# Kernel tuning notes

Hardware: AMD Instinct MI355X
Metric: run time of the kernel (lower is better)

The kernel has to match this reference:

```python
import jax, jax.numpy as jnp
import numpy as np
from jax import lax

B, L = 2048, 2048
CIN, CONV, D, NCLS = 1, 128, 1024, 1000
E, H, K = 6, 2 * 1024, 2  # num_experts, expert hidden, top-k


def setup_inputs() -> dict:
    key = jax.random.key(0)
    ks = jax.random.split(key, 16)
    s = lambda *sh: 0.02
    return {
        "x": jax.random.normal(ks[0], (B, L), jnp.float32),
        "conv1_w": jax.random.normal(ks[1], (CONV, CIN, 5), jnp.float32) * 0.1,
        "conv1_b": jnp.zeros((CONV,), jnp.float32),
        "conv2_w": jax.random.normal(ks[2], (CONV, CONV, 5), jnp.float32) * 0.05,
        "conv2_b": jnp.zeros((CONV,), jnp.float32),
        "proj_w": jax.random.normal(ks[3], (D, CONV), jnp.float32) * 0.05,
        "proj_b": jnp.zeros((D,), jnp.float32),
        "router_w": jax.random.normal(ks[4], (E, D), jnp.float32) * 0.02,
        "router_b": jnp.zeros((E,), jnp.float32),
        "exp_w1": jax.random.normal(ks[5], (E, H, D), jnp.float32) * 0.02,
        "exp_b1": jnp.zeros((E, H), jnp.float32),
        "exp_w2": jax.random.normal(ks[6], (E, D, H), jnp.float32) * 0.02,
        "exp_b2": jnp.zeros((E, D), jnp.float32),
        "cls_w": jax.random.normal(ks[7], (NCLS, D), jnp.float32) * 0.02,
        "cls_b": jnp.zeros((NCLS,), jnp.float32),
    }


def _conv1d(x, w, b):
    # x: [B, C, L]; torch Conv1d(k=5, stride=2, pad=2)
    y = lax.conv_general_dilated(x, w, window_strides=(2,), padding=[(2, 2)],
                                 dimension_numbers=("NCH", "OIH", "NCH"))
    return y + b[None, :, None]


def reference(x, conv1_w, conv1_b, conv2_w, conv2_b, proj_w, proj_b,
              router_w, router_b, exp_w1, exp_b1, exp_w2, exp_b2, cls_w, cls_b):
    h = x[:, None, :]                               # [B,1,L]
    h = jax.nn.relu(_conv1d(h, conv1_w, conv1_b))   # [B,CONV,L/2]
    h = jax.nn.relu(_conv1d(h, conv2_w, conv2_b))   # [B,CONV,L/4]
    h = h.mean(axis=-1)                             # [B,CONV]
    h = h @ proj_w.T + proj_b                       # [B,D]

    # Top-2 router
    probs = jax.nn.softmax(h @ router_w.T + router_b, axis=-1)  # [B,E]
    top_vals, top_idx = lax.top_k(probs, K)                     # [B,2]
    # per-token per-expert combine weights (exact same math as masked loop)
    combine = (jax.nn.one_hot(top_idx[:, 0], E, dtype=h.dtype) * top_vals[:, 0:1]
               + jax.nn.one_hot(top_idx[:, 1], E, dtype=h.dtype) * top_vals[:, 1:2])  # [B,E]

    # all-expert FFN, then masked combine (equivalent to gather/scatter dispatch)
    hid = jax.nn.relu(jnp.einsum("bd,ehd->beh", h, exp_w1) + exp_b1)  # [B,E,H]
    eo = jnp.einsum("beh,edh->bed", hid, exp_w2) + exp_b2             # [B,E,D]
    moe = jnp.einsum("be,bed->bd", combine, eo)                       # [B,D]

    return moe @ cls_w.T + cls_b                                      # [B,NCLS]
```

## Files before the change

### kernel.cpp

```cpp
#include <hip/hip_runtime.h>
#include <hip/hip_bf16.h>
#include <hip/hip_fp16.h>
#include <stdint.h>

#define BB 2048
#define LL 2048
#define CV 128
#define DD 1024
#define NC 1000
#define EE 6
#define HH 2048

typedef __bf16 bf16_t;
typedef _Float16 f16_t;
typedef __attribute__((ext_vector_type(8))) __bf16 bf16x8;
typedef __attribute__((ext_vector_type(8))) _Float16 f16x8;
typedef __attribute__((ext_vector_type(4))) _Float16 f16x4;
typedef __attribute__((ext_vector_type(4))) float f32x4;

__device__ __forceinline__ void gload_lds16(const void* g, void* l)
{
    __builtin_amdgcn_global_load_lds(
        (const __attribute__((address_space(1))) unsigned int*)g,
        (__attribute__((address_space(3))) unsigned int*)l, 16, 0, 0);
}

__global__ void k_prep_w2(const float* __restrict__ w2, bf16_t* __restrict__ wsw)
{
    int idx = blockIdx.x * 256 + threadIdx.x;
    if (idx >= 5 * 128 * 128) return;
    int kk = idx % 5;
    int t2 = idx / 5;
    int ci = t2 & 127;
    int co = t2 >> 7;
    float v = w2[idx];
    bf16_t h = (bf16_t)v;
    bf16_t l = (bf16_t)(v - (float)h);
    int cb = ci >> 5, j = ci & 31;
    int t  = cb * 5 + kk;
    int si = (co * 32 + j) ^ ((co & 7) << 3);
    wsw[(size_t)t * 8192 + si]        = h;
    wsw[(size_t)t * 8192 + 4096 + si] = l;
}

__global__ void k_prep_exp(const float* __restrict__ ew1, const float* __restrict__ ew2,
                           const float* __restrict__ cw,  f16_t* __restrict__ ew1h,
                           f16_t* __restrict__ ew2h, f16_t* __restrict__ clsh)
{
    const size_t n1 = (size_t)EE * HH * DD / 4;
    const size_t n2 = n1 + (size_t)EE * DD * HH / 4;
    const size_t n3 = n2 + (size_t)NC * DD / 4;
    size_t i4 = (size_t)blockIdx.x * 256 + threadIdx.x;
    if (i4 >= n3) return;
    const float* src; f16_t* dst; size_t off;
    if (i4 < n1)      { src = ew1; dst = ew1h; off = i4; }
    else if (i4 < n2) { src = ew2; dst = ew2h; off = i4 - n1; }
    else              { src = cw;  dst = clsh; off = i4 - n2; }
    float4 v = reinterpret_cast<const float4*>(src)[off];
    f16x4 r;
    r[0] = (f16_t)v.x; r[1] = (f16_t)v.y; r[2] = (f16_t)v.z; r[3] = (f16_t)v.w;
    reinterpret_cast<f16x4*>(dst)[off] = r;
}

__launch_bounds__(512, 2)
__global__ void k_conv(const float* __restrict__ x,  const float* __restrict__ w1,
                       const float* __restrict__ b1, const bf16_t* __restrict__ wsw,
                       const float* __restrict__ b2, float* __restrict__ hbar)
{
    __shared__ __align__(16) float w1s[640];
    __shared__ __align__(16) float b1s[128];
    __shared__ __align__(16) float b2s[128];
    __shared__ __align__(16) float red[8][64];
    __shared__ __align__(16) short h1s[2][2][8320];
    __shared__ __align__(16) short wlds[3 * 8192];

    const int tid  = threadIdx.x;
    const int b0   = blockIdx.x * 2;
    const int lane = tid & 63;
    const int wid  = tid >> 6;
    const int l15  = lane & 15, lg = lane >> 4;
    const int wb   = wid >> 2;
    const int wm   = (wid >> 1) & 1;
    const int wn   = wid & 1;
    const int gb   = tid >> 8;
    const int gtid = tid & 255;
    const int jo   = gtid & 3;
    const int rg   = gtid >> 2;

    for (int i = tid; i < 640; i += 512) w1s[i] = w1[i];
    if (tid < 128) { b1s[tid] = b1[tid]; b2s[tid] = b2[tid]; }

    const float* xrow = x + (size_t)(b0 + gb) * LL;
    const short* h1p  = &h1s[wb][0][0];

    float racc[4][4];
#pragma unroll
    for (int m = 0; m < 4; ++m)
#pragma unroll
        for (int r = 0; r < 4; ++r) racc[m][r] = 0.f;

#define KSTEP(kk, buf)                                                          \
    do {                                                                        \
        const short* wp = wlds + (buf) * 8192;                                  \
        bf16x8 ah[4], al[4], bh[4], bl[4];                                      \
        _Pragma("unroll")                                                       \
        for (int m = 0; m < 4; ++m) {                                           \
            int si = ((wm * 64 + m * 16 + l15) * 32 + lg * 8) ^ ((l15 & 7) << 3); \
            ah[m] = *reinterpret_cast<const bf16x8*>(wp + si);                  \
            al[m] = *reinterpret_cast<const bf16x8*>(wp + 4096 + si);           \
        }                                                                       \
        _Pragma("unroll")                                                       \
        for (int n = 0; n < 4; ++n) {                                           \
            int r = 2 * (wn * 64 + n * 16 + l15) + (kk);                        \
            int si = (r * 32 + lg * 8) ^ (((r >> 1) & 7) << 3);                 \
            bh[n] = *reinterpret_cast<const bf16x8*>(h1p + si);                 \
            bl[n] = *reinterpret_cast<const bf16x8*>(h1p + 8320 + si);          \
        }                                                                       \
        _Pragma("unroll")                                                       \
        for (int m = 0; m < 4; ++m)                                             \
            _Pragma("unroll")                                                   \
            for (int n = 0; n < 4; ++n)                                         \
                acc[m][n] = __builtin_amdgcn_mfma_f32_16x16x32_bf16(ah[m], bh[n], acc[m][n], 0, 0, 0); \
        _Pragma("unroll")                                                       \
        for (int m = 0; m < 4; ++m)                                             \
            _Pragma("unroll")                                                   \
            for (int n = 0; n < 4; ++n)                                         \
                acc[m][n] = __builtin_amdgcn_mfma_f32_16x16x32_bf16(ah[m], bl[n], acc[m][n], 0, 0, 0); \
        _Pragma("unroll")                                                       \
        for (int m = 0; m < 4; ++m)                                             \
            _Pragma("unroll")                                                   \
            for (int n = 0; n < 4; ++n)                                         \
                acc[m][n] = __builtin_amdgcn_mfma_f32_16x16x32_bf16(al[m], bh[n], acc[m][n], 0, 0, 0); \
    } while (0)

    for (int c = 0; c < 4; ++c) {
        const int t1base = 256 * c - 2;

        f32x4 acc[4][4];
#pragma unroll
        for (int m = 0; m < 4; ++m)
#pragma unroll
            for (int n = 0; n < 4; ++n)
#pragma unroll
                for (int r = 0; r < 4; ++r) acc[m][n][r] = 0.f;

        for (int cb = 0; cb < 4; ++cb) {
            __syncthreads();

            {
                const bf16_t* src = wsw + (size_t)cb * 40960;
#pragma unroll
                for (int j = 0; j < 6; ++j) {
                    int q = j * 512 + tid;
                    gload_lds16(src + q * 8, wlds + q * 8);
                }
            }

            const int ci0 = cb * 32 + jo * 8;
            float wf[40], br8[8];
#pragma unroll
            for (int q = 0; q < 10; ++q)
                *reinterpret_cast<float4*>(&wf[q * 4]) =
                    *reinterpret_cast<const float4*>(&w1s[ci0 * 5 + q * 4]);
            *reinterpret_cast<float4*>(&br8[0]) = *reinterpret_cast<const float4*>(&b1s[ci0]);
            *reinterpret_cast<float4*>(&br8[4]) = *reinterpret_cast<const float4*>(&b1s[ci0 + 4]);

#pragma unroll
            for (int it = 0; it < 5; ++it) {
                int r = rg + it * 64;
                if (it < 4 || r < 260) {
                    int t1 = t1base + r;
                    bool valid = (unsigned)t1 < 1024u;
                    float xv[5];
#pragma unroll
                    for (int kk = 0; kk < 5; ++kk) {
                        int xg = 2 * t1 - 2 + kk;
                        xv[kk] = (valid && (unsigned)xg < 2048u) ? xrow[xg] : 0.f;
                    }
                    bf16x8 hv, lv;
#pragma unroll
                    for (int u = 0; u < 8; ++u) {
                        float v = 0.f;
                        if (valid) {
                            v = br8[u];
#pragma unroll
                            for (int kk = 0; kk < 5; ++kk) v += wf[u * 5 + kk] * xv[kk];
                            v = fmaxf(v, 0.f);
                        }
                        bf16_t h = (bf16_t)v;
                        hv[u] = h;
                        lv[u] = (bf16_t)(v - (float)h);
                    }
                    int si = (r * 32 + jo * 8) ^ (((r >> 1) & 7) << 3);
                    *reinterpret_cast<bf16x8*>(&h1s[gb][0][si]) = hv;
                    *reinterpret_cast<bf16x8*>(&h1s[gb][1][si]) = lv;
                }
            }
            __syncthreads();

            KSTEP(0, 0);
            KSTEP(1, 1);
            __syncthreads();

            {
                const bf16_t* src = wsw + (size_t)cb * 40960 + 24576;
#pragma unroll
                for (int j = 0; j < 4; ++j) {
                    int q = j * 512 + tid;
                    gload_lds16(src + q * 8, wlds + q * 8);
                }
            }
            KSTEP(2, 2);
            __syncthreads();

            KSTEP(3, 0);
            KSTEP(4, 1);
        }
#pragma unroll
        for (int m = 0; m < 4; ++m)
#pragma unroll
            for (int r = 0; r < 4; ++r) {
                int co = wm * 64 + m * 16 + lg * 4 + r;
                float bias = b2s[co];
                float s = 0.f;
#pragma unroll
                for (int n = 0; n < 4; ++n) s += fmaxf(acc[m][n][r] + bias, 0.f);
                racc[m][r] += s;
            }
    }
#undef KSTEP

#pragma unroll
    for (int m = 0; m < 4; ++m)
#pragma unroll
        for (int r = 0; r < 4; ++r) {
            float v = racc[m][r];
            v += __shfl_xor(v, 1);
            v += __shfl_xor(v, 2);
            v += __shfl_xor(v, 4);
            v += __shfl_xor(v, 8);
            racc[m][r] = v;
        }
    if (l15 == 0) {
#pragma unroll
        for (int m = 0; m < 4; ++m)
#pragma unroll
            for (int r = 0; r < 4; ++r)
                red[wid][m * 16 + lg * 4 + r] = racc[m][r];
    }
    __syncthreads();
    if (tid < 256) {
        int wb2 = tid >> 7, cc = tid & 127;
        int wm2 = cc >> 6, loc = cc & 63;
        float s = red[wb2 * 4 + wm2 * 2 + 0][loc] + red[wb2 * 4 + wm2 * 2 + 1][loc];
        hbar[(size_t)(b0 + wb2) * 128 + cc] = s * (1.f / 512.f);
    }
}

__launch_bounds__(256)
__global__ void k_proj(const float* __restrict__ hbar, const float* __restrict__ pw,
                       const float* __restrict__ pb, float* __restrict__ h)
{
    __shared__ float hbs[64 * 128];
    const int tid = threadIdx.x;
    const int b0 = blockIdx.x * 64, d0 = blockIdx.y * 64;
    for (int i = tid * 4; i < 64 * 128; i += 1024)
        *reinterpret_cast<float4*>(&hbs[i]) =
            *reinterpret_cast<const float4*>(&hbar[(size_t)b0 * 128 + i]);
    __syncthreads();
    const int tx = tid & 15, ty = tid >> 4;
    float acc[4][4];
#pragma unroll
    for (int i = 0; i < 4; ++i)
#pragma unroll
        for (int j = 0; j < 4; ++j) acc[i][j] = 0.f;
    const float* pwr[4];
#pragma unroll
    for (int j = 0; j < 4; ++j) pwr[j] = pw + (size_t)(d0 + tx * 4 + j) * 128;
    for (int k = 0; k < 128; k += 4) {
        float4 wv[4], av[4];
#pragma unroll
        for (int j = 0; j < 4; ++j) wv[j] = *reinterpret_cast<const float4*>(pwr[j] + k);
#pragma unroll
        for (int i = 0; i < 4; ++i) av[i] = *reinterpret_cast<const float4*>(&hbs[(ty * 4 + i) * 128 + k]);
#pragma unroll
        for (int i = 0; i < 4; ++i)
#pragma unroll
            for (int j = 0; j < 4; ++j)
                acc[i][j] += av[i].x * wv[j].x + av[i].y * wv[j].y +
                             av[i].z * wv[j].z + av[i].w * wv[j].w;
    }
#pragma unroll
    for (int i = 0; i < 4; ++i) {
        int bb = b0 + ty * 4 + i;
#pragma unroll
        for (int j = 0; j < 4; ++j) {
            int d = d0 + tx * 4 + j;
            h[(size_t)bb * DD + d] = acc[i][j] + pb[d];
        }
    }
}

__launch_bounds__(256)
__global__ void k_router(const float* __restrict__ h, const float* __restrict__ rw,
                         const float* __restrict__ rb, float* __restrict__ comb,
                         int2* __restrict__ top)
{
    const int lane = threadIdx.x & 63;
    const int b = blockIdx.x * 4 + (threadIdx.x >> 6);
    float part[6] = {0.f, 0.f, 0.f, 0.f, 0.f, 0.f};
    for (int j = 0; j < 16; ++j) {
        int d = j * 64 + lane;
        float hv = h[(size_t)b * DD + d];
#pragma unroll
        for (int e = 0; e < 6; ++e) part[e] += rw[e * DD + d] * hv;
    }
#pragma unroll
    for (int e = 0; e < 6; ++e) {
        float v = part[e];
        for (int off = 32; off > 0; off >>= 1) v += __shfl_xor(v, off);
        part[e] = v;
    }
    if (lane == 0) {
        float lgt[6];
#pragma unroll
        for (int e = 0; e < 6; ++e) lgt[e] = part[e] + rb[e];
        int i1 = 0;
#pragma unroll
        for (int e = 1; e < 6; ++e) if (lgt[e] > lgt[i1]) i1 = e;
        int i2 = -1;
#pragma unroll
        for (int e = 0; e < 6; ++e)
            if (e != i1 && (i2 < 0 || lgt[e] > lgt[i2])) i2 = e;
        float mx = lgt[i1], s = 0.f, ex[6];
#pragma unroll
        for (int e = 0; e < 6; ++e) { ex[e] = expf(lgt[e] - mx); s += ex[e]; }
        float inv = 1.f / s;
#pragma unroll
        for (int e = 0; e < 6; ++e) comb[b * 8 + e] = 0.f;
        comb[b * 8 + 6] = 0.f; comb[b * 8 + 7] = 0.f;
        comb[b * 8 + i1] = ex[i1] * inv;
        comb[b * 8 + i2] = ex[i2] * inv;
        top[b] = make_int2(i1, i2);
    }
}

__global__ void k_index(const int2* __restrict__ top, int* __restrict__ meta,
                        int* __restrict__ idxg)
{
    __shared__ int wsum[4];
    const int tid = threadIdx.x, lane = tid & 63, wid = tid >> 6;
    int2 tk[8];
#pragma unroll
    for (int j = 0; j < 8; ++j) tk[j] = top[tid * 8 + j];
    int off_run = 0;
    for (int e = 0; e < 6; ++e) {
        int m[8], c = 0;
#pragma unroll
        for (int j = 0; j < 8; ++j) { m[j] = (tk[j].x == e || tk[j].y == e) ? 1 : 0; c += m[j]; }
        int v = c;
        for (int d = 1; d < 64; d <<= 1) { int u = __shfl_up(v, d); if (lane >= d) v += u; }
        if (lane == 63) wsum[wid] = v;
        __syncthreads();
        int wbase = 0;
#pragma unroll
        for (int w = 0; w < 4; ++w) if (w < wid) wbase += wsum[w];
        int total = wsum[0] + wsum[1] + wsum[2] + wsum[3];
        int p = off_run + wbase + (v - c);
#pragma unroll
        for (int j = 0; j < 8; ++j) if (m[j]) idxg[p++] = tid * 8 + j;
        if (tid == 0) { meta[e] = total; meta[8 + e] = off_run; }
        off_run += total;
        __syncthreads();
    }
    if (tid == 0) meta[14] = off_run;
}

__device__ inline f16x8 cvt8(const float4 a, const float4 b)
{
    f16x8 r;
    r[0] = (f16_t)a.x; r[1] = (f16_t)a.y; r[2] = (f16_t)a.z; r[3] = (f16_t)a.w;
    r[4] = (f16_t)b.x; r[5] = (f16_t)b.y; r[6] = (f16_t)b.z; r[7] = (f16_t)b.w;
    return r;
}

template<int EPI, int NFRAG>
__launch_bounds__(256, 3)
__global__ void k_moe(const float* __restrict__ hsrc, const f16_t* __restrict__ hidg,
                      const f16_t* __restrict__ eog, const float* __restrict__ Bp,
                      const f16_t* __restrict__ Bh, const float* __restrict__ bias,
                      f16_t* __restrict__ outH, f16_t* __restrict__ eogW,
                      float* __restrict__ outF, const float* __restrict__ comb,
                      const int2* __restrict__ top, const int* __restrict__ meta,
                      const int* __restrict__ idxg, int N, int K, int NCLIP)
{
    constexpr int BN = NFRAG * 32;
    __shared__ f16_t As[128 * 72];
    __shared__ f16_t Bs[BN * 72];
    const int tid = threadIdx.x;
    const int e  = blockIdx.z;
    const int m0 = blockIdx.x * 128, n0 = blockIdx.y * BN;
    int cnt = 1 << 30, off = 0;
    if (EPI != 3) {
        cnt = meta[e]; off = meta[8 + e];
        if (m0 >= cnt) return;
    }
    const int lane = tid & 63, wid = tid >> 6;
    const int l15 = lane & 15, lg = lane >> 4;
    const int wm = wid >> 1, wn = wid & 1;

    f32x4 acc[4][NFRAG];
#pragma unroll
    for (int i = 0; i < 4; ++i)
#pragma unroll
        for (int j = 0; j < NFRAG; ++j)
#pragma unroll
            for (int r = 0; r < 4; ++r) acc[i][j][r] = 0.f;

    for (int k0 = 0; k0 < K; k0 += 64) {
        __syncthreads();
        {
            const int row = tid >> 1, c0 = (tid & 1) * 32;
            f16x8* d = reinterpret_cast<f16x8*>(As + row * 72 + c0);
            if (EPI == 1) {
                int lr = m0 + row;
                int token = (lr < cnt) ? idxg[off + lr] : 0;
                const float4* s = reinterpret_cast<const float4*>(hsrc + (size_t)token * K + k0 + c0);
#pragma unroll
                for (int j = 0; j < 4; ++j) d[j] = cvt8(s[2 * j], s[2 * j + 1]);
            } else if (EPI == 2) {
                const uint4* s = reinterpret_cast<const uint4*>(hidg + (size_t)(off + m0 + row) * K + k0 + c0);
#pragma unroll
                for (int j = 0; j < 4; ++j) reinterpret_cast<uint4*>(d)[j] = s[j];
            } else {
                int r = m0 + row;
                const f16x8* s0 = reinterpret_cast<const f16x8*>(eog + ((size_t)r * 2) * K + k0 + c0);
                const f16x8* s1 = reinterpret_cast<const f16x8*>(eog + ((size_t)r * 2 + 1) * K + k0 + c0);
#pragma unroll
                for (int j = 0; j < 4; ++j) d[j] = s0[j] + s1[j];
            }
        }
        {
            constexpr int PERTHR = BN * 64 / 256;
            constexpr int TPR = 64 / PERTHR;
            const int row = tid / TPR, c0 = (tid % TPR) * PERTHR;
            const bool ok = (n0 + row) < NCLIP;
            f16x8* d = reinterpret_cast<f16x8*>(Bs + row * 72 + c0);
            if (Bh) {
                const uint4* s = reinterpret_cast<const uint4*>(
                    Bh + (size_t)e * N * K + (size_t)(n0 + row) * K + k0 + c0);
#pragma unroll
                for (int j = 0; j < PERTHR / 8; ++j) {
                    uint4 v = ok ? s[j] : make_uint4(0, 0, 0, 0);
                    reinterpret_cast<uint4*>(d)[j] = v;
                }
            } else {
                const float4* s = reinterpret_cast<const float4*>(
                    Bp + (size_t)e * N * K + (size_t)(n0 + row) * K + k0 + c0);
#pragma unroll
                for (int j = 0; j < PERTHR / 8; ++j) {
                    float4 a = ok ? s[2 * j]     : make_float4(0.f, 0.f, 0.f, 0.f);
                    float4 b = ok ? s[2 * j + 1] : make_float4(0.f, 0.f, 0.f, 0.f);
                    d[j] = cvt8(a, b);
                }
            }
        }
        __syncthreads();
#pragma unroll
        for (int kk = 0; kk < 64; kk += 32) {
            f16x8 af[4], bq[NFRAG];
#pragma unroll
            for (int i = 0; i < 4; ++i)
                af[i] = *reinterpret_cast<const f16x8*>(As + (wm * 64 + i * 16 + l15) * 72 + kk + lg * 8);
#pragma unroll
            for (int j = 0; j < NFRAG; ++j)
                bq[j] = *reinterpret_cast<const f16x8*>(Bs + (wn * (BN / 2) + j * 16 + l15) * 72 + kk + lg * 8);
#pragma unroll
            for (int i = 0; i < 4; ++i)
#pragma unroll
                for (int j = 0; j < NFRAG; ++j)
                    acc[i][j] = __builtin_amdgcn_mfma_f32_16x16x32_f16(af[i], bq[j], acc[i][j], 0, 0, 0);
        }
    }
#pragma unroll
    for (int i = 0; i < 4; ++i) {
#pragma unroll
        for (int j = 0; j < NFRAG; ++j) {
#pragma unroll
            for (int r = 0; r < 4; ++r) {
                int lr  = m0 + wm * 64 + i * 16 + lg * 4 + r;
                int col = n0 + wn * (BN / 2) + j * 16 + l15;
                float c = acc[i][j][r];
                if (EPI == 1) {
                    if (lr < cnt)
                        outH[(size_t)(off + lr) * N + col] = (f16_t)fmaxf(c + bias[(size_t)e * N + col], 0.f);
                } else if (EPI == 2) {
                    if (lr < cnt) {
                        int token = idxg[off + lr];
                        int slot = (top[token].x == e) ? 0 : 1;
                        float w = comb[token * 8 + e];
                        eogW[((size_t)token * 2 + slot) * N + col] = (f16_t)(w * (c + bias[(size_t)e * N + col]));
                    }
                } else {
                    if (col < NCLIP)
                        outF[(size_t)lr * NCLIP + col] = c + bias[col];
                }
            }
        }
    }
}

extern "C" void kernel_launch(void* const* d_in, const int* in_sizes, int n_in,
                              void* d_out, int out_size, void* d_ws, size_t ws_size,
                              hipStream_t stream)
{
    const float* x   = (const float*)d_in[0];
    const float* w1  = (const float*)d_in[1];
    const float* b1  = (const float*)d_in[2];
    const float* w2  = (const float*)d_in[3];
    const float* b2  = (const float*)d_in[4];
    const float* pw  = (const float*)d_in[5];
    const float* pb  = (const float*)d_in[6];
    const float* rw  = (const float*)d_in[7];
    const float* rb  = (const float*)d_in[8];
    const float* ew1 = (const float*)d_in[9];
    const float* eb1 = (const float*)d_in[10];
    const float* ew2 = (const float*)d_in[11];
    const float* eb2 = (const float*)d_in[12];
    const float* cw  = (const float*)d_in[13];
    const float* cb  = (const float*)d_in[14];
    float* out = (float*)d_out;

    char* ws = (char*)d_ws;
    bf16_t* wsw  = (bf16_t*)(ws + 0);
    float*  hbar = (float*)(ws + 327680);
    float*  h    = (float*)(ws + 1376256);
    f16_t*  eog  = (f16_t*)(ws + 1376256);
    float*  comb = (float*)(ws + 9764864);
    int2*   top  = (int2*)(ws + 9830400);
    int*    meta = (int*)(ws + 9846784);
    int*    idxg = (int*)(ws + 9847040);
    f16_t*  hidg = (f16_t*)(ws + 9863424);
    f16_t*  ew1h = (f16_t*)(ws + 27164928);
    f16_t*  ew2h = (f16_t*)(ws + 52330752);
    f16_t*  clsh = (f16_t*)(ws + 77496576);

    const bool f16w = ws_size >= 79593728ull;

    k_prep_w2<<<320, 256, 0, stream>>>(w2, wsw);
    if (f16w)
        k_prep_exp<<<25576, 256, 0, stream>>>(ew1, ew2, cw, ew1h, ew2h, clsh);
    k_conv<<<1024, 512, 0, stream>>>(x, w1, b1, wsw, b2, hbar);
    k_proj<<<dim3(32, 16), 256, 0, stream>>>(hbar, pw, pb, h);
    k_router<<<512, 256, 0, stream>>>(h, rw, rb, comb, top);
    k_index<<<1, 256, 0, stream>>>(top, meta, idxg);
    k_moe<1, 4><<<dim3(16, 16, 6), 256, 0, stream>>>(
        h, nullptr, nullptr, ew1, f16w ? ew1h : nullptr, eb1,
        hidg, nullptr, nullptr, comb, top, meta, idxg, HH, DD, HH);
    k_moe<2, 4><<<dim3(16, 8, 6), 256, 0, stream>>>(
        nullptr, hidg, nullptr, ew2, f16w ? ew2h : nullptr, eb2,
        nullptr, eog, nullptr, comb, top, meta, idxg, DD, HH, DD);
    k_moe<3, 2><<<dim3(16, 16, 1), 256, 0, stream>>>(
        nullptr, nullptr, eog, cw, f16w ? clsh : nullptr, cb,
        nullptr, nullptr, out, comb, top, meta, idxg, DD, DD, NC);
}
```

Before: 731.1 us.

## Switch conv2 MFMA to 32x32x16 tiles and stage input rows in LDS

The conv2 GEMM inside k_conv moves from 16x16x32 bf16 MFMA to 32x32x16 bf16 MFMA. Fragment loads, accumulator layout, the bias/ReLU/mean epilogue and the cross-lane reduction are remapped to fit the new tile shape. The input row chunk for each c-iteration is now loaded once into shared memory, so the conv1 stage reads x from LDS instead of doing repeated guarded global loads. The change adds LDS usage and reworks index mapping, which risks layout mistakes and changes in register pressure.

New measurement: 758.5 us. 1.04x slower.

```diff
diff --git a/kernel.cpp b/kernel.cpp
--- a/kernel.cpp
+++ b/kernel.cpp
@@ -17,6 +17,7 @@
 typedef __attribute__((ext_vector_type(8))) _Float16 f16x8;
 typedef __attribute__((ext_vector_type(4))) _Float16 f16x4;
 typedef __attribute__((ext_vector_type(4))) float f32x4;
+typedef __attribute__((ext_vector_type(16))) float f32x16;
 
 __device__ __forceinline__ void gload_lds16(const void* g, void* l)
 {
@@ -71,6 +72,7 @@
     __shared__ __align__(16) float b1s[128];
     __shared__ __align__(16) float b2s[128];
     __shared__ __align__(16) float red[8][64];
+    __shared__ __align__(16) float xs[2][528];
     __shared__ __align__(16) short h1s[2][2][8320];
     __shared__ __align__(16) short wlds[3 * 8192];
 
@@ -78,7 +80,8 @@
     const int b0   = blockIdx.x * 2;
     const int lane = tid & 63;
     const int wid  = tid >> 6;
-    const int l15  = lane & 15, lg = lane >> 4;
+    const int l31  = lane & 31;
+    const int lh   = lane >> 5;
     const int wb   = wid >> 2;
     const int wm   = (wid >> 1) & 1;
     const int wn   = wid & 1;
@@ -90,59 +93,83 @@
     for (int i = tid; i < 640; i += 512) w1s[i] = w1[i];
     if (tid < 128) { b1s[tid] = b1[tid]; b2s[tid] = b2[tid]; }
 
-    const float* xrow = x + (size_t)(b0 + gb) * LL;
-    const short* h1p  = &h1s[wb][0][0];
-
-    float racc[4][4];
-#pragma unroll
-    for (int m = 0; m < 4; ++m)
-#pragma unroll
-        for (int r = 0; r < 4; ++r) racc[m][r] = 0.f;
+    const short* h1p = &h1s[wb][0][0];
+
+    float racc[2][16];
+#pragma unroll
+    for (int m = 0; m < 2; ++m)
+#pragma unroll
+        for (int g = 0; g < 16; ++g) racc[m][g] = 0.f;
 
 #define KSTEP(kk, buf)                                                          \
     do {                                                                        \
         const short* wp = wlds + (buf) * 8192;                                  \
-        bf16x8 ah[4], al[4], bh[4], bl[4];                                      \
+        bf16x8 ah[2][2], al[2][2], bh[2][2], bl[2][2];                          \
         _Pragma("unroll")                                                       \
-        for (int m = 0; m < 4; ++m) {                                           \
-            int si = ((wm * 64 + m * 16 + l15) * 32 + lg * 8) ^ ((l15 & 7) << 3); \
-            ah[m] = *reinterpret_cast<const bf16x8*>(wp + si);                  \
-            al[m] = *reinterpret_cast<const bf16x8*>(wp + 4096 + si);           \
+        for (int m = 0; m < 2; ++m) {                                           \
+            int co = wm * 64 + m * 32 + l31;                                    \
+            _Pragma("unroll")                                                   \
+            for (int kh = 0; kh < 2; ++kh) {                                    \
+                int si = (co * 32 + kh * 16 + lh * 8) ^ ((co & 7) << 3);        \
+                ah[m][kh] = *reinterpret_cast<const bf16x8*>(wp + si);          \
+                al[m][kh] = *reinterpret_cast<const bf16x8*>(wp + 4096 + si);   \
+            }                                                                   \
         }                                                                       \
         _Pragma("unroll")                                                       \
-        for (int n = 0; n < 4; ++n) {                                           \
-            int r = 2 * (wn * 64 + n * 16 + l15) + (kk);                        \
-            int si = (r * 32 + lg * 8) ^ (((r >> 1) & 7) << 3);                 \
-            bh[n] = *reinterpret_cast<const bf16x8*>(h1p + si);                 \
-            bl[n] = *reinterpret_cast<const bf16x8*>(h1p + 8320 + si);          \
+        for (int n = 0; n < 2; ++n) {                                           \
+            int r = 2 * (wn * 64 + n * 32 + l31) + (kk);                        \
+            _Pragma("unroll")                                                   \
+            for (int kh = 0; kh < 2; ++kh) {                                    \
+                int si = (r * 32 + kh * 16 + lh * 8) ^ (((r >> 1) & 7) << 3);   \
+                bh[n][kh] = *reinterpret_cast<const bf16x8*>(h1p + si);         \
+                bl[n][kh] = *reinterpret_cast<const bf16x8*>(h1p + 8320 + si);  \
+            }                                                                   \
         }                                                                       \
         _Pragma("unroll")                                                       \
-        for (int m = 0; m < 4; ++m)                                             \
+        for (int kh = 0; kh < 2; ++kh)                                          \
             _Pragma("unroll")                                                   \
-            for (int n = 0; n < 4; ++n)                                         \
-                acc[m][n] = __builtin_amdgcn_mfma_f32_16x16x32_bf16(ah[m], bh[n], acc[m][n], 0, 0, 0); \
+            for (int m = 0; m < 2; ++m)                                         \
+                _Pragma("unroll")                                               \
+                for (int n = 0; n < 2; ++n)                                     \
+                    acc[m][n] = __builtin_amdgcn_mfma_f32_32x32x16_bf16(ah[m][kh], bh[n][kh], acc[m][n], 0, 0, 0); \
         _Pragma("unroll")                                                       \
-        for (int m = 0; m < 4; ++m)                                             \
+        for (int kh = 0; kh < 2; ++kh)                                          \
             _Pragma("unroll")                                                   \
-            for (int n = 0; n < 4; ++n)                                         \
-                acc[m][n] = __builtin_amdgcn_mfma_f32_16x16x32_bf16(ah[m], bl[n], acc[m][n], 0, 0, 0); \
+            for (int m = 0; m < 2; ++m)                                         \
+                _Pragma("unroll")                                               \
+                for (int n = 0; n < 2; ++n)                                     \
+                    acc[m][n] = __builtin_amdgcn_mfma_f32_32x32x16_bf16(ah[m][kh], bl[n][kh], acc[m][n], 0, 0, 0); \
         _Pragma("unroll")                                                       \
-        for (int m = 0; m < 4; ++m)                                             \
+        for (int kh = 0; kh < 2; ++kh)                                          \
             _Pragma("unroll")                                                   \
-            for (int n = 0; n < 4; ++n)                                         \
-                acc[m][n] = __builtin_amdgcn_mfma_f32_16x16x32_bf16(al[m], bh[n], acc[m][n], 0, 0, 0); \
+            for (int m = 0; m < 2; ++m)                                         \
+                _Pragma("unroll")                                               \
+                for (int n = 0; n < 2; ++n)                                     \
+                    acc[m][n] = __builtin_amdgcn_mfma_f32_32x32x16_bf16(al[m][kh], bh[n][kh], acc[m][n], 0, 0, 0); \
     } while (0)
 
     for (int c = 0; c < 4; ++c) {
         const int t1base = 256 * c - 2;
 
-        f32x4 acc[4][4];
-#pragma unroll
-        for (int m = 0; m < 4; ++m)
-#pragma unroll
-            for (int n = 0; n < 4; ++n)
-#pragma unroll
-                for (int r = 0; r < 4; ++r) acc[m][n][r] = 0.f;
+        {
+            const int xoff = 512 * c - 6;
+            for (int i = tid; i < 1056; i += 512) {
+                int batch = (i >= 528) ? 1 : 0;
+                int idx = i - batch * 528;
+                int xg = xoff + idx;
+                float v = ((unsigned)xg < 2048u)
+                              ? x[(size_t)(b0 + batch) * LL + xg] : 0.f;
+                xs[batch][idx] = v;
+            }
+        }
+
+        f32x16 acc[2][2];
+#pragma unroll
+        for (int m = 0; m < 2; ++m)
+#pragma unroll
+            for (int n = 0; n < 2; ++n)
+#pragma unroll
+                for (int g = 0; g < 16; ++g) acc[m][n][g] = 0.f;
 
         for (int cb = 0; cb < 4; ++cb) {
             __syncthreads();
@@ -169,24 +196,17 @@
             for (int it = 0; it < 5; ++it) {
                 int r = rg + it * 64;
                 if (it < 4 || r < 260) {
-                    int t1 = t1base + r;
-                    bool valid = (unsigned)t1 < 1024u;
+                    bool valid = (unsigned)(t1base + r) < 1024u;
                     float xv[5];
 #pragma unroll
-                    for (int kk = 0; kk < 5; ++kk) {
-                        int xg = 2 * t1 - 2 + kk;
-                        xv[kk] = (valid && (unsigned)xg < 2048u) ? xrow[xg] : 0.f;
-                    }
+                    for (int kk = 0; kk < 5; ++kk) xv[kk] = xs[gb][2 * r + kk];
                     bf16x8 hv, lv;
 #pragma unroll
                     for (int u = 0; u < 8; ++u) {
-                        float v = 0.f;
-                        if (valid) {
-                            v = br8[u];
-#pragma unroll
-                            for (int kk = 0; kk < 5; ++kk) v += wf[u * 5 + kk] * xv[kk];
-                            v = fmaxf(v, 0.f);
-                        }
+                        float v = br8[u];
+#pragma unroll
+                        for (int kk = 0; kk < 5; ++kk) v += wf[u * 5 + kk] * xv[kk];
+                        v = valid ? fmaxf(v, 0.f) : 0.f;
                         bf16_t h = (bf16_t)v;
                         hv[u] = h;
                         lv[u] = (bf16_t)(v - (float)h);
@@ -217,36 +237,38 @@
             KSTEP(4, 1);
         }
 #pragma unroll
-        for (int m = 0; m < 4; ++m)
-#pragma unroll
-            for (int r = 0; r < 4; ++r) {
-                int co = wm * 64 + m * 16 + lg * 4 + r;
-                float bias = b2s[co];
-                float s = 0.f;
-#pragma unroll
-                for (int n = 0; n < 4; ++n) s += fmaxf(acc[m][n][r] + bias, 0.f);
-                racc[m][r] += s;
+        for (int m = 0; m < 2; ++m)
+#pragma unroll
+            for (int g = 0; g < 16; ++g) {
+                int co_l = m * 32 + (g & 3) + 8 * (g >> 2) + 4 * lh;
+                float bias = b2s[wm * 64 + co_l];
+                racc[m][g] += fmaxf(acc[m][0][g] + bias, 0.f)
+                            + fmaxf(acc[m][1][g] + bias, 0.f);
             }
     }
 #undef KSTEP
 
-#pragma unroll
-    for (int m = 0; m < 4; ++m)
-#pragma unroll
-        for (int r = 0; r < 4; ++r) {
-            float v = racc[m][r];
+    asm volatile("s_waitcnt vmcnt(0)" ::: "memory");
+    __syncthreads();
+
+#pragma unroll
+    for (int m = 0; m < 2; ++m)
+#pragma unroll
+        for (int g = 0; g < 16; ++g) {
+            float v = racc[m][g];
             v += __shfl_xor(v, 1);
             v += __shfl_xor(v, 2);
             v += __shfl_xor(v, 4);
             v += __shfl_xor(v, 8);
-            racc[m][r] = v;
-        }
-    if (l15 == 0) {
-#pragma unroll
-        for (int m = 0; m < 4; ++m)
-#pragma unroll
-            for (int r = 0; r < 4; ++r)
-                red[wid][m * 16 + lg * 4 + r] = racc[m][r];
+            v += __shfl_xor(v, 16);
+            racc[m][g] = v;
+        }
+    if (l31 == 0) {
+#pragma unroll
+        for (int m = 0; m < 2; ++m)
+#pragma unroll
+            for (int g = 0; g < 16; ++g)
+                red[wid][m * 32 + (g & 3) + 8 * (g >> 2) + 4 * lh] = racc[m][g];
     }
     __syncthreads();
     if (tid < 256) {
```

## Load conv2 weight fragments directly from global into registers, one batch per block

Applied to the files above, without the earlier changes.

The conv kernel now processes one batch row per 256-thread block instead of two rows per 512-thread block. The conv2 weight tiles are no longer staged in LDS through async global-to-LDS copies. Each wave instead reads its A fragments straight from global/L2 into registers, double-buffered across the five kernel taps, which removes several block barriers and frees LDS. The input row segment is also staged in LDS so conv1 no longer does repeated bounds-checked global loads. In exchange, weight reuse across waves now relies on the L2 cache rather than shared memory, and register pressure rises from holding two sets of fragments.

After: 723.0 us. No clear change (-1.1%).

```diff
diff --git a/kernel.cpp b/kernel.cpp
--- a/kernel.cpp
+++ b/kernel.cpp
@@ -17,13 +17,6 @@
 typedef __attribute__((ext_vector_type(8))) _Float16 f16x8;
 typedef __attribute__((ext_vector_type(4))) _Float16 f16x4;
 typedef __attribute__((ext_vector_type(4))) float f32x4;
-
-__device__ __forceinline__ void gload_lds16(const void* g, void* l)
-{
-    __builtin_amdgcn_global_load_lds(
-        (const __attribute__((address_space(1))) unsigned int*)g,
-        (__attribute__((address_space(3))) unsigned int*)l, 16, 0, 0);
-}
 
 __global__ void k_prep_w2(const float* __restrict__ w2, bf16_t* __restrict__ wsw)
 {
@@ -36,11 +29,10 @@
     float v = w2[idx];
     bf16_t h = (bf16_t)v;
     bf16_t l = (bf16_t)(v - (float)h);
-    int cb = ci >> 5, j = ci & 31;
-    int t  = cb * 5 + kk;
-    int si = (co * 32 + j) ^ ((co & 7) << 3);
-    wsw[(size_t)t * 8192 + si]        = h;
-    wsw[(size_t)t * 8192 + 4096 + si] = l;
+    int t = (ci >> 5) * 5 + kk;
+    int j = ci & 31;
+    wsw[(size_t)t * 8192 + co * 32 + j]        = h;
+    wsw[(size_t)t * 8192 + 4096 + co * 32 + j] = l;
 }
 
 __global__ void k_prep_exp(const float* __restrict__ ew1, const float* __restrict__ ew2,
@@ -62,7 +54,7 @@
     reinterpret_cast<f16x4*>(dst)[off] = r;
 }
 
-__launch_bounds__(512, 2)
+__launch_bounds__(256, 2)
 __global__ void k_conv(const float* __restrict__ x,  const float* __restrict__ w1,
                        const float* __restrict__ b1, const bf16_t* __restrict__ wsw,
                        const float* __restrict__ b2, float* __restrict__ hbar)
@@ -70,28 +62,24 @@
     __shared__ __align__(16) float w1s[640];
     __shared__ __align__(16) float b1s[128];
     __shared__ __align__(16) float b2s[128];
-    __shared__ __align__(16) float red[8][64];
-    __shared__ __align__(16) short h1s[2][2][8320];
-    __shared__ __align__(16) short wlds[3 * 8192];
+    __shared__ __align__(16) float red[4][64];
+    __shared__ __align__(16) float xs[528];
+    __shared__ __align__(16) short h1s[2][8320];
 
     const int tid  = threadIdx.x;
-    const int b0   = blockIdx.x * 2;
+    const int b    = blockIdx.x;
     const int lane = tid & 63;
     const int wid  = tid >> 6;
     const int l15  = lane & 15, lg = lane >> 4;
-    const int wb   = wid >> 2;
-    const int wm   = (wid >> 1) & 1;
-    const int wn   = wid & 1;
-    const int gb   = tid >> 8;
-    const int gtid = tid & 255;
-    const int jo   = gtid & 3;
-    const int rg   = gtid >> 2;
-
-    for (int i = tid; i < 640; i += 512) w1s[i] = w1[i];
+    const int wm   = wid >> 1,  wn = wid & 1;
+    const int jo   = tid & 3;
+    const int rg   = tid >> 2;
+
+    for (int i = tid; i < 640; i += 256) w1s[i] = w1[i];
     if (tid < 128) { b1s[tid] = b1[tid]; b2s[tid] = b2[tid]; }
 
-    const float* xrow = x + (size_t)(b0 + gb) * LL;
-    const short* h1p  = &h1s[wb][0][0];
+    const float* xrow = x + (size_t)b * LL;
+    const int aoff = (wm * 64 + l15) * 32 + lg * 8;
 
     float racc[4][4];
 #pragma unroll
@@ -99,43 +87,54 @@
 #pragma unroll
         for (int r = 0; r < 4; ++r) racc[m][r] = 0.f;
 
-#define KSTEP(kk, buf)                                                          \
+#define PREF(T, AH, AL)                                                         \
     do {                                                                        \
-        const short* wp = wlds + (buf) * 8192;                                  \
-        bf16x8 ah[4], al[4], bh[4], bl[4];                                      \
+        const bf16_t* wp_ = wsw + (size_t)(T) * 8192 + aoff;                    \
         _Pragma("unroll")                                                       \
         for (int m = 0; m < 4; ++m) {                                           \
-            int si = ((wm * 64 + m * 16 + l15) * 32 + lg * 8) ^ ((l15 & 7) << 3); \
-            ah[m] = *reinterpret_cast<const bf16x8*>(wp + si);                  \
-            al[m] = *reinterpret_cast<const bf16x8*>(wp + 4096 + si);           \
+            AH[m] = *reinterpret_cast<const bf16x8*>(wp_ + m * 512);            \
+            AL[m] = *reinterpret_cast<const bf16x8*>(wp_ + 4096 + m * 512);     \
         }                                                                       \
+    } while (0)
+
+#define KSTEP(kk, AH, AL)                                                       \
+    do {                                                                        \
+        bf16x8 bh[4], bl[4];                                                    \
         _Pragma("unroll")                                                       \
         for (int n = 0; n < 4; ++n) {                                           \
             int r = 2 * (wn * 64 + n * 16 + l15) + (kk);                        \
             int si = (r * 32 + lg * 8) ^ (((r >> 1) & 7) << 3);                 \
-            bh[n] = *reinterpret_cast<const bf16x8*>(h1p + si);                 \
-            bl[n] = *reinterpret_cast<const bf16x8*>(h1p + 8320 + si);          \
+            bh[n] = *reinterpret_cast<const bf16x8*>(&h1s[0][si]);              \
+            bl[n] = *reinterpret_cast<const bf16x8*>(&h1s[1][si]);              \
         }                                                                       \
         _Pragma("unroll")                                                       \
         for (int m = 0; m < 4; ++m)                                             \
             _Pragma("unroll")                                                   \
             for (int n = 0; n < 4; ++n)                                         \
-                acc[m][n] = __builtin_amdgcn_mfma_f32_16x16x32_bf16(ah[m], bh[n], acc[m][n], 0, 0, 0); \
+                acc[m][n] = __builtin_amdgcn_mfma_f32_16x16x32_bf16(AH[m], bh[n], acc[m][n], 0, 0, 0); \
         _Pragma("unroll")                                                       \
         for (int m = 0; m < 4; ++m)                                             \
             _Pragma("unroll")                                                   \
             for (int n = 0; n < 4; ++n)                                         \
-                acc[m][n] = __builtin_amdgcn_mfma_f32_16x16x32_bf16(ah[m], bl[n], acc[m][n], 0, 0, 0); \
+                acc[m][n] = __builtin_amdgcn_mfma_f32_16x16x32_bf16(AH[m], bl[n], acc[m][n], 0, 0, 0); \
         _Pragma("unroll")                                                       \
         for (int m = 0; m < 4; ++m)                                             \
             _Pragma("unroll")                                                   \
             for (int n = 0; n < 4; ++n)                                         \
-                acc[m][n] = __builtin_amdgcn_mfma_f32_16x16x32_bf16(al[m], bh[n], acc[m][n], 0, 0, 0); \
+                acc[m][n] = __builtin_amdgcn_mfma_f32_16x16x32_bf16(AL[m], bh[n], acc[m][n], 0, 0, 0); \
     } while (0)
 
     for (int c = 0; c < 4; ++c) {
         const int t1base = 256 * c - 2;
 
+        {
+            const int xoff = 512 * c - 6;
+            for (int i = tid; i < 528; i += 256) {
+                int xg = xoff + i;
+                xs[i] = ((unsigned)xg < 2048u) ? xrow[xg] : 0.f;
+            }
+        }
+
         f32x4 acc[4][4];
 #pragma unroll
         for (int m = 0; m < 4; ++m)
@@ -147,14 +146,8 @@
         for (int cb = 0; cb < 4; ++cb) {
             __syncthreads();
 
-            {
-                const bf16_t* src = wsw + (size_t)cb * 40960;
-#pragma unroll
-                for (int j = 0; j < 6; ++j) {
-                    int q = j * 512 + tid;
-                    gload_lds16(src + q * 8, wlds + q * 8);
-                }
-            }
+            bf16x8 ah0[4], al0[4], ah1[4], al1[4];
+            PREF(cb * 5 + 0, ah0, al0);
 
             const int ci0 = cb * 32 + jo * 8;
             float wf[40], br8[8];
@@ -169,52 +162,37 @@
             for (int it = 0; it < 5; ++it) {
                 int r = rg + it * 64;
                 if (it < 4 || r < 260) {
-                    int t1 = t1base + r;
-                    bool valid = (unsigned)t1 < 1024u;
+                    bool valid = (unsigned)(t1base + r) < 1024u;
                     float xv[5];
 #pragma unroll
-                    for (int kk = 0; kk < 5; ++kk) {
-                        int xg = 2 * t1 - 2 + kk;
-                        xv[kk] = (valid && (unsigned)xg < 2048u) ? xrow[xg] : 0.f;
-                    }
+                    for (int kk = 0; kk < 5; ++kk) xv[kk] = xs[2 * r + kk];
                     bf16x8 hv, lv;
 #pragma unroll
                     for (int u = 0; u < 8; ++u) {
-                        float v = 0.f;
-                        if (valid) {
-                            v = br8[u];
-#pragma unroll
-                            for (int kk = 0; kk < 5; ++kk) v += wf[u * 5 + kk] * xv[kk];
-                            v = fmaxf(v, 0.f);
-                        }
+                        float v = br8[u];
+#pragma unroll
+                        for (int kk = 0; kk < 5; ++kk) v += wf[u * 5 + kk] * xv[kk];
+                        v = valid ? fmaxf(v, 0.f) : 0.f;
                         bf16_t h = (bf16_t)v;
                         hv[u] = h;
                         lv[u] = (bf16_t)(v - (float)h);
                     }
                     int si = (r * 32 + jo * 8) ^ (((r >> 1) & 7) << 3);
-                    *reinterpret_cast<bf16x8*>(&h1s[gb][0][si]) = hv;
-                    *reinterpret_cast<bf16x8*>(&h1s[gb][1][si]) = lv;
+                    *reinterpret_cast<bf16x8*>(&h1s[0][si]) = hv;
+                    *reinterpret_cast<bf16x8*>(&h1s[1][si]) = lv;
                 }
             }
             __syncthreads();
 
-            KSTEP(0, 0);
-            KSTEP(1, 1);
-            __syncthreads();
-
-            {
-                const bf16_t* src = wsw + (size_t)cb * 40960 + 24576;
-#pragma unroll
-                for (int j = 0; j < 4; ++j) {
-                    int q = j * 512 + tid;
-                    gload_lds16(src + q * 8, wlds + q * 8);
-                }
-            }
-            KSTEP(2, 2);
-            __syncthreads();
-
-            KSTEP(3, 0);
-            KSTEP(4, 1);
+            PREF(cb * 5 + 1, ah1, al1);
+            KSTEP(0, ah0, al0);
+            PREF(cb * 5 + 2, ah0, al0);
+            KSTEP(1, ah1, al1);
+            PREF(cb * 5 + 3, ah1, al1);
+            KSTEP(2, ah0, al0);
+            PREF(cb * 5 + 4, ah0, al0);
+            KSTEP(3, ah1, al1);
+            KSTEP(4, ah0, al0);
         }
 #pragma unroll
         for (int m = 0; m < 4; ++m)
@@ -229,6 +207,7 @@
             }
     }
 #undef KSTEP
+#undef PREF
 
 #pragma unroll
     for (int m = 0; m < 4; ++m)
@@ -241,6 +220,7 @@
             v += __shfl_xor(v, 8);
             racc[m][r] = v;
         }
+    __syncthreads();
     if (l15 == 0) {
 #pragma unroll
         for (int m = 0; m < 4; ++m)
@@ -249,11 +229,10 @@
                 red[wid][m * 16 + lg * 4 + r] = racc[m][r];
     }
     __syncthreads();
-    if (tid < 256) {
-        int wb2 = tid >> 7, cc = tid & 127;
-        int wm2 = cc >> 6, loc = cc & 63;
-        float s = red[wb2 * 4 + wm2 * 2 + 0][loc] + red[wb2 * 4 + wm2 * 2 + 1][loc];
-        hbar[(size_t)(b0 + wb2) * 128 + cc] = s * (1.f / 512.f);
+    if (tid < 128) {
+        int wm2 = tid >> 6, loc = tid & 63;
+        float s = red[wm2 * 2 + 0][loc] + red[wm2 * 2 + 1][loc];
+        hbar[(size_t)b * 128 + tid] = s * (1.f / 512.f);
     }
 }
 
@@ -550,7 +529,7 @@
     k_prep_w2<<<320, 256, 0, stream>>>(w2, wsw);
     if (f16w)
         k_prep_exp<<<25576, 256, 0, stream>>>(ew1, ew2, cw, ew1h, ew2h, clsh);
-    k_conv<<<1024, 512, 0, stream>>>(x, w1, b1, wsw, b2, hbar);
+    k_conv<<<2048, 256, 0, stream>>>(x, w1, b1, wsw, b2, hbar);
     k_proj<<<dim3(32, 16), 256, 0, stream>>>(hbar, pw, pb, h);
     k_router<<<512, 256, 0, stream>>>(h, rw, rb, comb, top);
     k_index<<<1, 256, 0, stream>>>(top, meta, idxg);
```
